# Optimization experiments

Hardware: AMD Instinct MI355X
Metric: run time of the kernel (lower is better)

The kernel has to match this reference:

```python
import math
import jax, jax.numpy as jnp
import numpy as np

B, Q, L, H = 32, 40, 1024, 1024
WINDOW_FRAMES, MAX_V_L = 16, 1024
MAX_DELTA = 0.1
NUM_PASSES = 2


def setup_inputs() -> dict:
    key = jax.random.key(0)
    ks = jax.random.split(key, 8)
    init_log_sigma = math.log(WINDOW_FRAMES / (2.0 * MAX_V_L))
    return {
        "pred_spans": jax.random.uniform(ks[0], (B, Q, 2), dtype=jnp.float32),
        "vid_feat": jax.random.normal(ks[1], (B, L, H), dtype=jnp.float32),
        "vid_mask": jnp.ones((B, L), dtype=jnp.float32),
        "txt_rep": jax.random.normal(ks[2], (B, H), dtype=jnp.float32),
        "log_sigma_start": jnp.float32(init_log_sigma),
        "log_sigma_end": jnp.float32(init_log_sigma),
        "sigma_width_scale_start": jnp.float32(0.01),
        "sigma_width_scale_end": jnp.float32(-0.01),
        "txt_proj_w": jax.random.normal(ks[3], (H, 2), dtype=jnp.float32) * 0.02,
        "txt_proj_b": jnp.zeros((2,), dtype=jnp.float32),
        "mlp0_w": jax.random.normal(ks[4], (3 * H, H), dtype=jnp.float32) * (1.0 / math.sqrt(3 * H)),
        "mlp0_b": jnp.zeros((H,), dtype=jnp.float32),
        "mlp1_w": jax.random.normal(ks[5], (H, 2), dtype=jnp.float32) * (1.0 / math.sqrt(H)),
        "mlp1_b": jnp.zeros((2,), dtype=jnp.float32),
    }


def reference(pred_spans, vid_feat, vid_mask, txt_rep,
              log_sigma_start, log_sigma_end,
              sigma_width_scale_start, sigma_width_scale_end,
              txt_proj_w, txt_proj_b, mlp0_w, mlp0_b, mlp1_w, mlp1_b):
    b, q, _ = pred_spans.shape
    l = vid_feat.shape[1]
    # span (center,width) -> (start,end) in [0,1]
    start = jnp.clip(pred_spans[..., 0] - pred_spans[..., 1] / 2, 0.0, 1.0)  # (B,Q)
    end = jnp.clip(pred_spans[..., 0] + pred_spans[..., 1] / 2, 0.0, 1.0)
    t_pos = jnp.linspace(0.0, 1.0, l)  # (L,)
    min_sig = 1.0 / (4.0 * l)
    log_range = math.log(max(float(l) * min_sig * 4.0, 1.0 + 1e-6))
    # semantic sigma offsets (B,2)
    txt_off = jnp.tanh(txt_rep @ txt_proj_w + txt_proj_b) * (0.5 * log_range)
    txt_off_s, txt_off_e = txt_off[:, 0:1], txt_off[:, 1:2]  # (B,1)
    txt_expand = jnp.broadcast_to(txt_rep[:, None, :], (b, q, txt_rep.shape[-1]))
    mask = vid_mask[:, None, :]  # (B,1,L)

    def _pool(anchor, sigma):
        # Gaussian soft-attention pooling over frames; anchor,sigma: (B,Q)
        dist2 = ((t_pos[None, None, :] - anchor[:, :, None]) / sigma[:, :, None]) ** 2
        w = jnp.exp(-0.5 * dist2) * mask  # (B,Q,L)
        w = w / jnp.maximum(jnp.sum(w, -1, keepdims=True), 1e-8)
        return jnp.einsum('bql,blh->bqh', w, vid_feat)

    passes = []
    for _ in range(NUM_PASSES):
        width = jnp.maximum(end - start, 1e-6)  # (B,Q)
        sig_s = jnp.maximum(jnp.exp(log_sigma_start + sigma_width_scale_start * width + txt_off_s), min_sig)
        sig_e = jnp.maximum(jnp.exp(log_sigma_end + sigma_width_scale_end * width + txt_off_e), min_sig)
        start_feat = _pool(start, sig_s)
        end_feat = _pool(end, sig_e)
        joint = jnp.concatenate([start_feat, end_feat, txt_expand], axis=-1)  # (B,Q,3H)
        hidden = jax.nn.relu(joint @ mlp0_w + mlp0_b)
        deltas = jnp.tanh(hidden @ mlp1_w + mlp1_b) * MAX_DELTA  # (B,Q,2)
        start = jnp.clip(start + deltas[..., 0], 0.0, 1.0)
        end = jnp.clip(end + deltas[..., 1], 0.0, 1.0)
        center_r = (start + end) / 2.0
        width_r = jnp.maximum(end - start, 1e-6)
        passes.append(jnp.stack([center_r, width_r], axis=-1))
    return passes[-1], jnp.stack(passes, axis=0)
```

## Files before the change

### kernel.cpp

```cpp
#include <hip/hip_runtime.h>

#define B_   32
#define Q_   40
#define L_   1024
#define H_   1024
#define QQ_  80
#define M_   1280
#define K3_  3072
#define JK_  2048

#define OB_W0T   0u
#define OB_WT2   6291456u
#define OB_JOINT 11534336u
#define OB_PART  16777216u
#define OB_TXTB  27262976u
#define OB_TXTP  27328512u
#define OB_MISC  27590656u
#define MS_START 0
#define MS_END   1280
#define MS_TOS   2560
#define MS_TOE   2592

typedef short bf8 __attribute__((ext_vector_type(8)));
typedef short bf4 __attribute__((ext_vector_type(4)));
typedef float f4  __attribute__((ext_vector_type(4)));

static __device__ __forceinline__ unsigned short f2b(float f) {
    unsigned int x = __float_as_uint(f);
    unsigned int r = x + 0x7FFFu + ((x >> 16) & 1u);
    return (unsigned short)(r >> 16);
}
static __device__ __forceinline__ unsigned int pk2(float lo, float hi) {
    return (unsigned int)f2b(lo) | ((unsigned int)f2b(hi) << 16);
}
static __device__ __forceinline__ float b2f16(unsigned short u) {
    return __uint_as_float((unsigned int)u << 16);
}
static __device__ __forceinline__ float blo(unsigned int u) {
    return __uint_as_float(u << 16);
}
static __device__ __forceinline__ float bhi(unsigned int u) {
    return __uint_as_float(u & 0xffff0000u);
}

static __device__ __forceinline__ void block_reduce2(float& a, float& b, float* scr) {
    #pragma unroll
    for (int off = 32; off > 0; off >>= 1) {
        a += __shfl_down(a, off);
        b += __shfl_down(b, off);
    }
    int wv = threadIdx.x >> 6, lane = threadIdx.x & 63;
    __syncthreads();
    if (lane == 0) { scr[wv] = a; scr[4 + wv] = b; }
    __syncthreads();
    a = scr[0] + scr[1] + scr[2] + scr[3];
    b = scr[4] + scr[5] + scr[6] + scr[7];
}

__global__ __launch_bounds__(256) void k_setup(const float* __restrict__ w0,
                                               unsigned short* __restrict__ w0t,
                                               const float* __restrict__ txt,
                                               const float* __restrict__ pw,
                                               const float* __restrict__ pb,
                                               const float* __restrict__ spans,
                                               unsigned short* __restrict__ txtb,
                                               float* __restrict__ msc) {
    int z = blockIdx.z, tid = threadIdx.x;
    if (z == 3) {
        int flat = blockIdx.x * 16 + blockIdx.y;
        if (flat < B_) {
            int b = flat;
            int h4 = tid * 4;
            float4 tv = *(const float4*)(txt + (size_t)b * H_ + h4);
            float4 pa = *(const float4*)(pw + 2 * h4);
            float4 pc = *(const float4*)(pw + 2 * h4 + 4);
            float s0 = tv.x * pa.x + tv.y * pa.z + tv.z * pc.x + tv.w * pc.z;
            float s1 = tv.x * pa.y + tv.y * pa.w + tv.z * pc.y + tv.w * pc.w;
            ushort4 o;
            o.x = f2b(tv.x); o.y = f2b(tv.y); o.z = f2b(tv.z); o.w = f2b(tv.w);
            *(ushort4*)(txtb + (size_t)b * H_ + h4) = o;
            __shared__ float scr[8];
            block_reduce2(s0, s1, scr);
            if (tid == 0) {
                const float half_lr = 4.9999975e-07f;
                msc[MS_TOS + b] = tanhf(s0 + pb[0]) * half_lr;
                msc[MS_TOE + b] = tanhf(s1 + pb[1]) * half_lr;
            }
        } else if (flat < 37) {
            int i = (flat - B_) * 256 + tid;
            if (i < M_) {
                float c = spans[2 * i], w = spans[2 * i + 1];
                msc[MS_START + i] = fminf(fmaxf(c - 0.5f * w, 0.f), 1.f);
                msc[MS_END + i]   = fminf(fmaxf(c + 0.5f * w, 0.f), 1.f);
            }
        }
        return;
    }
    __shared__ float tile[64][69];
    const float* s = w0 + (size_t)z * 1024 * H_;
    unsigned short* d = w0t + (size_t)z * 1024;
    int r0 = blockIdx.x * 64, c0 = blockIdx.y * 64;
    int col4 = (tid & 15) * 4, row = tid >> 4;
    #pragma unroll
    for (int it = 0; it < 4; it++) {
        int r = it * 16 + row;
        float4 v = *(const float4*)(s + (size_t)(r0 + r) * 1024 + c0 + col4);
        *(float4*)(&tile[r][col4]) = v;
    }
    __syncthreads();
    #pragma unroll
    for (int it = 0; it < 2; it++) {
        int slot = it * 256 + tid;
        int c = slot >> 3, chunk = slot & 7;
        int r = chunk * 8;
        uint4 vv;
        vv.x = (unsigned int)f2b(tile[r + 0][c]) | ((unsigned int)f2b(tile[r + 1][c]) << 16);
        vv.y = (unsigned int)f2b(tile[r + 2][c]) | ((unsigned int)f2b(tile[r + 3][c]) << 16);
        vv.z = (unsigned int)f2b(tile[r + 4][c]) | ((unsigned int)f2b(tile[r + 5][c]) << 16);
        vv.w = (unsigned int)f2b(tile[r + 6][c]) | ((unsigned int)f2b(tile[r + 7][c]) << 16);
        *(uint4*)(d + (size_t)(c0 + c) * K3_ + r0 + r) = vv;
    }
}

static __device__ __forceinline__ void weights_body(int m, float s, float e,
                                                    const float* __restrict__ vmask,
                                                    float ls_s, float ls_e,
                                                    float sw_s, float sw_e,
                                                    const float* __restrict__ msc,
                                                    unsigned short* __restrict__ wt2,
                                                    float* scr) {
    int b = m / Q_, q = m - b * Q_;
    int tid = threadIdx.x;
    float width = fmaxf(e - s, 1e-6f);
    const float min_sig = 1.0f / (4.0f * (float)L_);
    float sig_s = fmaxf(expf(ls_s + sw_s * width + msc[MS_TOS + b]), min_sig);
    float sig_e = fmaxf(expf(ls_e + sw_e * width + msc[MS_TOE + b]), min_sig);
    float inv_s = 1.0f / sig_s, inv_e = 1.0f / sig_e;

    float wsv[4], wev[4], sumS = 0.f, sumE = 0.f;
    #pragma unroll
    for (int k = 0; k < 4; k++) {
        int l = tid + k * 256;
        float t = (float)l * (1.0f / 1023.0f);
        float mk = vmask[b * L_ + l];
        float ds = (t - s) * inv_s, de = (t - e) * inv_e;
        float a = expf(-0.5f * ds * ds) * mk;
        float c = expf(-0.5f * de * de) * mk;
        wsv[k] = a; wev[k] = c; sumS += a; sumE += c;
    }
    block_reduce2(sumS, sumE, scr);
    float iS = 1.0f / fmaxf(sumS, 1e-8f);
    float iE = 1.0f / fmaxf(sumE, 1e-8f);
    unsigned short* wq = wt2 + ((size_t)b * QQ_ + q) * L_;
    unsigned short* we = wt2 + ((size_t)b * QQ_ + Q_ + q) * L_;
    #pragma unroll
    for (int k = 0; k < 4; k++) {
        int l = tid + k * 256;
        wq[l] = f2b(wsv[k] * iS);
        we[l] = f2b(wev[k] * iE);
    }
}

__global__ __launch_bounds__(256) void k_stage2(const float* __restrict__ vmask,
                                                const float* __restrict__ p_ls_s,
                                                const float* __restrict__ p_ls_e,
                                                const float* __restrict__ p_sw_s,
                                                const float* __restrict__ p_sw_e,
                                                const float* __restrict__ msc,
                                                unsigned short* __restrict__ wt2,
                                                const unsigned short* __restrict__ txtb,
                                                const unsigned short* __restrict__ w0t,
                                                unsigned short* __restrict__ txtp) {
    int bid = blockIdx.x;
    if (bid < M_) {
        __shared__ float scr[8];
        int m = bid;
        weights_body(m, msc[MS_START + m], msc[MS_END + m], vmask,
                     p_ls_s[0], p_ls_e[0], p_sw_s[0], p_sw_e[0], msc, wt2, scr);
        return;
    }
    int t = bid - M_;
    int nIdx = t & 15, mIdx = (t >> 4) & 1, kIdx = t >> 5;
    int wv = threadIdx.x >> 6, lane = threadIdx.x & 63;
    int ml = lane & 15, kg = lane >> 4;
    int mbase = mIdx * 16;
    int nbase = nIdx * 64 + wv * 16;
    int kz = kIdx * 256;
    const unsigned short* ap = txtb + ((size_t)(mbase + ml) * H_ + kz + kg * 8);
    const unsigned short* bp = w0t + ((size_t)(nbase + ml) * K3_ + JK_ + kz + kg * 8);
    f4 acc = (f4){0.f, 0.f, 0.f, 0.f};
    #pragma unroll
    for (int k0 = 0; k0 < 256; k0 += 32) {
        bf8 a = *(const bf8*)(ap + k0);
        bf8 bb = *(const bf8*)(bp + k0);
        acc = __builtin_amdgcn_mfma_f32_16x16x32_bf16(a, bb, acc, 0, 0, 0);
    }
    unsigned short* pp = txtp + (size_t)kIdx * B_ * H_;
    int n = nbase + ml;
    #pragma unroll
    for (int r = 0; r < 4; r++) {
        int m = mbase + kg * 4 + r;
        pp[(size_t)m * H_ + n] = f2b(acc[r]);
    }
}

__global__ __launch_bounds__(512) void k_pool_mfma(const float* __restrict__ vid,
                                                   const unsigned short* __restrict__ wt2,
                                                   unsigned short* __restrict__ joint) {
    int b = blockIdx.x, ht = blockIdx.y;
    int tid = threadIdx.x;
    int wv = tid >> 6, lane = tid & 63;
    int hsub = wv & 3, half = wv >> 2;
    int ml = lane & 15, kg = lane >> 4;
    int h0 = ht * 64;

    __shared__ __align__(16) unsigned short tb[2][2][2048];
    __shared__ __align__(16) unsigned short ta[2][2][80 * 40];
    __shared__ float cmb[80][68];

    int st = tid & 255;
    int sl = st >> 3;
    int sh8 = (st & 7) * 8;
    int b_off = ((((sh8 >> 4) * 2 + ((sl >> 2) & 1)) * 4 + (sl >> 3)) * 4 + (sl & 3)) * 16
                + (sh8 & 15);
    const float* vbase = vid + ((size_t)b * L_ + half * 512) * H_ + h0;
    const unsigned short* awsrc = wt2 + (size_t)b * QQ_ * L_ + half * 512;

    f4 acc[5];
    #pragma unroll
    for (int t = 0; t < 5; t++) acc[t] = (f4){0.f, 0.f, 0.f, 0.f};

    auto stage = [&](int c, int buf) {
        const float* src = vbase + (size_t)(c * 32 + sl) * H_ + sh8;
        float4 v0 = *(const float4*)(src);
        float4 v1 = *(const float4*)(src + 4);
        uint4 w;
        w.x = pk2(v0.x, v0.y);
        w.y = pk2(v0.z, v0.w);
        w.z = pk2(v1.x, v1.y);
        w.w = pk2(v1.z, v1.w);
        *(uint4*)(&tb[half][buf][b_off]) = w;
        {
            int row = st >> 2, seg = (st & 3) * 8;
            uint4 av = *(const uint4*)(awsrc + (size_t)row * L_ + c * 32 + seg);
            *(uint4*)(&ta[half][buf][row * 40 + seg]) = av;
        }
        if (st < 64) {
            int i = st + 256;
            int row = i >> 2, seg = (i & 3) * 8;
            uint4 av = *(const uint4*)(awsrc + (size_t)row * L_ + c * 32 + seg);
            *(uint4*)(&ta[half][buf][row * 40 + seg]) = av;
        }
    };

    stage(0, 0);
    __syncthreads();

    for (int c = 0; c < 16; c++) {
        int buf = c & 1;
        if (c < 15) stage(c + 1, buf ^ 1);

        unsigned trb = (unsigned)(uintptr_t)(&tb[half][buf][0]) + hsub * 1024 + lane * 8;
        bf4 lo, hi;
        asm volatile("ds_read_b64_tr_b16 %0, %2\n\t"
                     "ds_read_b64_tr_b16 %1, %2 offset:512\n\t"
                     "s_waitcnt lgkmcnt(0)"
                     : "=v"(lo), "=v"(hi)
                     : "v"(trb));
        __builtin_amdgcn_sched_barrier(0);
        bf8 bfrag = __builtin_shufflevector(lo, hi, 0, 1, 2, 3, 4, 5, 6, 7);

        #pragma unroll
        for (int t = 0; t < 5; t++) {
            bf8 afr = *(const bf8*)(&ta[half][buf][(t * 16 + ml) * 40 + kg * 8]);
            acc[t] = __builtin_amdgcn_mfma_f32_16x16x32_bf16(afr, bfrag, acc[t], 0, 0, 0);
        }
        __syncthreads();
    }

    if (half == 1) {
        #pragma unroll
        for (int t = 0; t < 5; t++)
            #pragma unroll
            for (int r = 0; r < 4; r++)
                cmb[t * 16 + kg * 4 + r][hsub * 16 + ml] = acc[t][r];
    }
    __syncthreads();
    if (half == 0) {
        #pragma unroll
        for (int t = 0; t < 5; t++)
            #pragma unroll
            for (int r = 0; r < 4; r++)
                cmb[t * 16 + kg * 4 + r][hsub * 16 + ml] += acc[t][r];
    }
    __syncthreads();
    for (int idx = tid; idx < 640; idx += 512) {
        int qq = idx >> 3, h8 = (idx & 7) * 8;
        const float* cr = &cmb[qq][h8];
        uint4 vv;
        vv.x = pk2(cr[0], cr[1]);
        vv.y = pk2(cr[2], cr[3]);
        vv.z = pk2(cr[4], cr[5]);
        vv.w = pk2(cr[6], cr[7]);
        int row = b * Q_ + (qq >= Q_ ? qq - Q_ : qq);
        int col = (qq >= Q_ ? H_ : 0) + h0 + h8;
        *(uint4*)(joint + (size_t)row * JK_ + col) = vv;
    }
}

__global__ __launch_bounds__(256) void k_mlp0_mfma(const unsigned short* __restrict__ joint,
                                                   const unsigned short* __restrict__ w0t,
                                                   const unsigned short* __restrict__ txtp,
                                                   unsigned short* __restrict__ part) {
    int wv = threadIdx.x >> 6, lane = threadIdx.x & 63;
    int ml = lane & 15, kg = lane >> 4;
    int mbase = blockIdx.x * 64 + wv * 16;
    int nbase = blockIdx.y * 64;
    int kbase = blockIdx.z * 512;
    const unsigned short* ap = joint + ((size_t)(mbase + ml) * JK_ + kbase + kg * 8);
    const unsigned short* bp = w0t + ((size_t)(nbase + ml) * K3_ + kbase + kg * 8);
    f4 acc[4];
    #pragma unroll
    for (int t = 0; t < 4; t++) acc[t] = (f4){0.f, 0.f, 0.f, 0.f};

    #pragma unroll 4
    for (int k0 = 0; k0 < 512; k0 += 32) {
        bf8 a = *(const bf8*)(ap + k0);
        #pragma unroll
        for (int t = 0; t < 4; t++) {
            bf8 bb = *(const bf8*)(bp + (size_t)t * 16 * K3_ + k0);
            acc[t] = __builtin_amdgcn_mfma_f32_16x16x32_bf16(a, bb, acc[t], 0, 0, 0);
        }
    }
    const unsigned short* tp = txtp + (size_t)blockIdx.z * B_ * H_;
    unsigned short* pp = part + (size_t)blockIdx.z * M_ * H_;
    #pragma unroll
    for (int t = 0; t < 4; t++) {
        int n = nbase + t * 16 + ml;
        #pragma unroll
        for (int r = 0; r < 4; r++) {
            int m = mbase + kg * 4 + r;
            int b = m / Q_;
            float v = acc[t][r] + b2f16(tp[(size_t)b * H_ + n]);
            pp[(size_t)m * H_ + n] = f2b(v);
        }
    }
}

__global__ __launch_bounds__(256) void k_mlp1w(const float* __restrict__ w1,
                                               const float* __restrict__ b0,
                                               const float* __restrict__ b1,
                                               const unsigned short* __restrict__ part,
                                               float* __restrict__ msc,
                                               float* __restrict__ out, int pass,
                                               int do_weights,
                                               const float* __restrict__ vmask,
                                               const float* __restrict__ p_ls_s,
                                               const float* __restrict__ p_ls_e,
                                               const float* __restrict__ p_sw_s,
                                               const float* __restrict__ p_sw_e,
                                               unsigned short* __restrict__ wt2) {
    int m = blockIdx.x, tid = threadIdx.x;
    int k4 = tid * 4;
    float4 bb = *(const float4*)(b0 + k4);
    float h0 = bb.x, h1 = bb.y, h2 = bb.z, h3 = bb.w;
    #pragma unroll
    for (int z = 0; z < 4; z++) {
        uint2 u = *(const uint2*)(part + (size_t)z * M_ * H_ + (size_t)m * H_ + k4);
        h0 += blo(u.x); h1 += bhi(u.x);
        h2 += blo(u.y); h3 += bhi(u.y);
    }
    h0 = fmaxf(h0, 0.f); h1 = fmaxf(h1, 0.f);
    h2 = fmaxf(h2, 0.f); h3 = fmaxf(h3, 0.f);
    float4 wa = *(const float4*)(w1 + 2 * k4);
    float4 wb = *(const float4*)(w1 + 2 * k4 + 4);
    float p0 = h0 * wa.x + h1 * wa.z + h2 * wb.x + h3 * wb.z;
    float p1 = h0 * wa.y + h1 * wa.w + h2 * wb.y + h3 * wb.w;

    __shared__ float scr[8];
    __shared__ float sh_s, sh_e;
    block_reduce2(p0, p1, scr);
    if (tid == 0) {
        float d0 = tanhf(p0 + b1[0]) * 0.1f;
        float d1 = tanhf(p1 + b1[1]) * 0.1f;
        float s = fminf(fmaxf(msc[MS_START + m] + d0, 0.f), 1.f);
        float e = fminf(fmaxf(msc[MS_END + m] + d1, 0.f), 1.f);
        msc[MS_START + m] = s;
        msc[MS_END + m] = e;
        sh_s = s; sh_e = e;
        float cen = 0.5f * (s + e);
        float wid = fmaxf(e - s, 1e-6f);
        out[2560 + (size_t)(pass * M_ + m) * 2 + 0] = cen;
        out[2560 + (size_t)(pass * M_ + m) * 2 + 1] = wid;
        if (pass == 1) { out[2 * m + 0] = cen; out[2 * m + 1] = wid; }
    }
    __syncthreads();
    if (do_weights) {
        weights_body(m, sh_s, sh_e, vmask,
                     p_ls_s[0], p_ls_e[0], p_sw_s[0], p_sw_e[0], msc, wt2, scr);
    }
}

extern "C" void kernel_launch(void* const* d_in, const int* in_sizes, int n_in,
                              void* d_out, int out_size, void* d_ws, size_t ws_size,
                              hipStream_t stream) {
    const float* spans = (const float*)d_in[0];
    const float* vid   = (const float*)d_in[1];
    const float* vmask = (const float*)d_in[2];
    const float* txt   = (const float*)d_in[3];
    const float* ls_s  = (const float*)d_in[4];
    const float* ls_e  = (const float*)d_in[5];
    const float* sw_s  = (const float*)d_in[6];
    const float* sw_e  = (const float*)d_in[7];
    const float* pw    = (const float*)d_in[8];
    const float* pb    = (const float*)d_in[9];
    const float* w0    = (const float*)d_in[10];
    const float* b0    = (const float*)d_in[11];
    const float* w1    = (const float*)d_in[12];
    const float* b1    = (const float*)d_in[13];
    char* wsb = (char*)d_ws;
    unsigned short* w0t   = (unsigned short*)(wsb + OB_W0T);
    unsigned short* wt2   = (unsigned short*)(wsb + OB_WT2);
    unsigned short* joint = (unsigned short*)(wsb + OB_JOINT);
    unsigned short* part  = (unsigned short*)(wsb + OB_PART);
    unsigned short* txtb  = (unsigned short*)(wsb + OB_TXTB);
    unsigned short* txtp  = (unsigned short*)(wsb + OB_TXTP);
    float* msc = (float*)(wsb + OB_MISC);
    float* out = (float*)d_out;

    hipLaunchKernelGGL(k_setup, dim3(16, 16, 4), dim3(256), 0, stream,
                       w0, w0t, txt, pw, pb, spans, txtb, msc);
    hipLaunchKernelGGL(k_stage2, dim3(M_ + 128), dim3(256), 0, stream,
                       vmask, ls_s, ls_e, sw_s, sw_e, msc, wt2, txtb, w0t, txtp);
    for (int p = 0; p < 2; p++) {
        hipLaunchKernelGGL(k_pool_mfma, dim3(B_, 16), dim3(512), 0, stream, vid, wt2, joint);
        hipLaunchKernelGGL(k_mlp0_mfma, dim3(20, 16, 4), dim3(256), 0, stream,
                           joint, w0t, txtp, part);
        hipLaunchKernelGGL(k_mlp1w, dim3(M_), dim3(256), 0, stream,
                           w1, b0, b1, part, msc, out, p, (p == 0) ? 1 : 0,
                           vmask, ls_s, ls_e, sw_s, sw_e, wt2);
    }
}
```

Before: 364.0 us.

## Restructure pooling kernel to single K-split with register-prefetched 64-frame chunks

The pooling GEMM drops the two-half K split across 512 threads in favour of 256 threads that each cover the full L dimension, using 64-frame chunks. Global loads for the next chunk go into registers before the MFMAs and are written to LDS afterwards, so memory latency overlaps compute. This also removes the shared-memory cross-half reduction and its extra barriers, writing results straight from the accumulators. The trade-off is fewer waves per block for hiding latency, more registers per thread, and uncoalesced scalar bf16 stores to joint.

```diff
diff --git a/kernel.cpp b/kernel.cpp
--- a/kernel.cpp
+++ b/kernel.cpp
@@ -204,107 +204,108 @@
     }
 }
 
-__global__ __launch_bounds__(512) void k_pool_mfma(const float* __restrict__ vid,
+__global__ __launch_bounds__(256) void k_pool_mfma(const float* __restrict__ vid,
                                                    const unsigned short* __restrict__ wt2,
                                                    unsigned short* __restrict__ joint) {
     int b = blockIdx.x, ht = blockIdx.y;
     int tid = threadIdx.x;
-    int wv = tid >> 6, lane = tid & 63;
-    int hsub = wv & 3, half = wv >> 2;
+    int hsub = tid >> 6, lane = tid & 63;
     int ml = lane & 15, kg = lane >> 4;
     int h0 = ht * 64;
 
-    __shared__ __align__(16) unsigned short tb[2][2][2048];
-    __shared__ __align__(16) unsigned short ta[2][2][80 * 40];
-    __shared__ float cmb[80][68];
-
-    int st = tid & 255;
-    int sl = st >> 3;
-    int sh8 = (st & 7) * 8;
-    int b_off = ((((sh8 >> 4) * 2 + ((sl >> 2) & 1)) * 4 + (sl >> 3)) * 4 + (sl & 3)) * 16
-                + (sh8 & 15);
-    const float* vbase = vid + ((size_t)b * L_ + half * 512) * H_ + h0;
-    const unsigned short* awsrc = wt2 + (size_t)b * QQ_ * L_ + half * 512;
+    __shared__ __align__(16) unsigned short tb[2][4096];
+    __shared__ __align__(16) unsigned short ta[2][80 * 72];
+
+    int l0 = tid >> 3;
+    int h8 = (tid & 7) * 8;
+    int sB = (l0 >> 2) & 1, kgB = l0 >> 3, lrB = l0 & 3;
+    int h16 = h8 >> 4, hc = h8 & 15;
+    int b_off = ((((h16) * 2 + sB) * 4 + kgB) * 64) + lrB * 16 + hc;
+    const float* vbase = vid + (size_t)b * L_ * H_ + h0 + h8;
+
+    const unsigned short* awsrc = wt2 + (size_t)b * QQ_ * L_;
 
     f4 acc[5];
     #pragma unroll
     for (int t = 0; t < 5; t++) acc[t] = (f4){0.f, 0.f, 0.f, 0.f};
 
-    auto stage = [&](int c, int buf) {
-        const float* src = vbase + (size_t)(c * 32 + sl) * H_ + sh8;
-        float4 v0 = *(const float4*)(src);
-        float4 v1 = *(const float4*)(src + 4);
+    float4 pv0, pv1, pv2, pv3;
+    uint4 av0, av1, av2;
+
+    auto issueB = [&](int c) {
+        const float* src = vbase + (size_t)(c * 64 + l0) * H_;
+        pv0 = *(const float4*)(src);
+        pv1 = *(const float4*)(src + 4);
+        pv2 = *(const float4*)(src + 32 * H_);
+        pv3 = *(const float4*)(src + 32 * H_ + 4);
+    };
+    auto issueA = [&](int c) {
+        int i0 = tid, i1 = tid + 256;
+        av0 = *(const uint4*)(awsrc + (size_t)(i0 >> 3) * L_ + c * 64 + (i0 & 7) * 8);
+        av1 = *(const uint4*)(awsrc + (size_t)(i1 >> 3) * L_ + c * 64 + (i1 & 7) * 8);
+        if (tid < 128) {
+            int i2 = tid + 512;
+            av2 = *(const uint4*)(awsrc + (size_t)(i2 >> 3) * L_ + c * 64 + (i2 & 7) * 8);
+        }
+    };
+    auto writeStage = [&](int buf) {
         uint4 w;
-        w.x = pk2(v0.x, v0.y);
-        w.y = pk2(v0.z, v0.w);
-        w.z = pk2(v1.x, v1.y);
-        w.w = pk2(v1.z, v1.w);
-        *(uint4*)(&tb[half][buf][b_off]) = w;
-        {
-            int row = st >> 2, seg = (st & 3) * 8;
-            uint4 av = *(const uint4*)(awsrc + (size_t)row * L_ + c * 32 + seg);
-            *(uint4*)(&ta[half][buf][row * 40 + seg]) = av;
-        }
-        if (st < 64) {
-            int i = st + 256;
-            int row = i >> 2, seg = (i & 3) * 8;
-            uint4 av = *(const uint4*)(awsrc + (size_t)row * L_ + c * 32 + seg);
-            *(uint4*)(&ta[half][buf][row * 40 + seg]) = av;
+        w.x = pk2(pv0.x, pv0.y); w.y = pk2(pv0.z, pv0.w);
+        w.z = pk2(pv1.x, pv1.y); w.w = pk2(pv1.z, pv1.w);
+        *(uint4*)(&tb[buf][b_off]) = w;
+        uint4 w2;
+        w2.x = pk2(pv2.x, pv2.y); w2.y = pk2(pv2.z, pv2.w);
+        w2.z = pk2(pv3.x, pv3.y); w2.w = pk2(pv3.z, pv3.w);
+        *(uint4*)(&tb[buf][b_off + 2048]) = w2;
+        int i0 = tid, i1 = tid + 256;
+        *(uint4*)(&ta[buf][(i0 >> 3) * 72 + (i0 & 7) * 8]) = av0;
+        *(uint4*)(&ta[buf][(i1 >> 3) * 72 + (i1 & 7) * 8]) = av1;
+        if (tid < 128) {
+            int i2 = tid + 512;
+            *(uint4*)(&ta[buf][(i2 >> 3) * 72 + (i2 & 7) * 8]) = av2;
         }
     };
 
-    stage(0, 0);
+    issueB(0); issueA(0);
+    writeStage(0);
     __syncthreads();
 
     for (int c = 0; c < 16; c++) {
         int buf = c & 1;
-        if (c < 15) stage(c + 1, buf ^ 1);
-
-        unsigned trb = (unsigned)(uintptr_t)(&tb[half][buf][0]) + hsub * 1024 + lane * 8;
-        bf4 lo, hi;
-        asm volatile("ds_read_b64_tr_b16 %0, %2\n\t"
-                     "ds_read_b64_tr_b16 %1, %2 offset:512\n\t"
-                     "s_waitcnt lgkmcnt(0)"
-                     : "=v"(lo), "=v"(hi)
-                     : "v"(trb));
-        __builtin_amdgcn_sched_barrier(0);
-        bf8 bfrag = __builtin_shufflevector(lo, hi, 0, 1, 2, 3, 4, 5, 6, 7);
+        if (c < 15) { issueB(c + 1); issueA(c + 1); }
 
         #pragma unroll
-        for (int t = 0; t < 5; t++) {
-            bf8 afr = *(const bf8*)(&ta[half][buf][(t * 16 + ml) * 40 + kg * 8]);
-            acc[t] = __builtin_amdgcn_mfma_f32_16x16x32_bf16(afr, bfrag, acc[t], 0, 0, 0);
-        }
+        for (int s2 = 0; s2 < 2; s2++) {
+            unsigned trb = (unsigned)(uintptr_t)(&tb[buf][0]) + (s2 * 4 + hsub) * 1024
+                           + lane * 8;
+            bf4 lo, hi;
+            asm volatile("ds_read_b64_tr_b16 %0, %2\n\t"
+                         "ds_read_b64_tr_b16 %1, %2 offset:512\n\t"
+                         "s_waitcnt lgkmcnt(0)"
+                         : "=v"(lo), "=v"(hi)
+                         : "v"(trb));
+            __builtin_amdgcn_sched_barrier(0);
+            bf8 bfrag = __builtin_shufflevector(lo, hi, 0, 1, 2, 3, 4, 5, 6, 7);
+            #pragma unroll
+            for (int t = 0; t < 5; t++) {
+                bf8 afr = *(const bf8*)(&ta[buf][(t * 16 + ml) * 72 + s2 * 32 + kg * 8]);
+                acc[t] = __builtin_amdgcn_mfma_f32_16x16x32_bf16(afr, bfrag, acc[t], 0, 0, 0);
+            }
+        }
+
+        if (c < 15) writeStage(buf ^ 1);
         __syncthreads();
     }
 
-    if (half == 1) {
+    #pragma unroll
+    for (int t = 0; t < 5; t++) {
         #pragma unroll
-        for (int t = 0; t < 5; t++)
-            #pragma unroll
-            for (int r = 0; r < 4; r++)
-                cmb[t * 16 + kg * 4 + r][hsub * 16 + ml] = acc[t][r];
-    }
-    __syncthreads();
-    if (half == 0) {
-        #pragma unroll
-        for (int t = 0; t < 5; t++)
-            #pragma unroll
-            for (int r = 0; r < 4; r++)
-                cmb[t * 16 + kg * 4 + r][hsub * 16 + ml] += acc[t][r];
-    }
-    __syncthreads();
-    for (int idx = tid; idx < 640; idx += 512) {
-        int qq = idx >> 3, h8 = (idx & 7) * 8;
-        const float* cr = &cmb[qq][h8];
-        uint4 vv;
-        vv.x = pk2(cr[0], cr[1]);
-        vv.y = pk2(cr[2], cr[3]);
-        vv.z = pk2(cr[4], cr[5]);
-        vv.w = pk2(cr[6], cr[7]);
-        int row = b * Q_ + (qq >= Q_ ? qq - Q_ : qq);
-        int col = (qq >= Q_ ? H_ : 0) + h0 + h8;
-        *(uint4*)(joint + (size_t)row * JK_ + col) = vv;
+        for (int r = 0; r < 4; r++) {
+            int qq = t * 16 + kg * 4 + r;
+            int row = b * Q_ + (qq >= Q_ ? qq - Q_ : qq);
+            int col = (qq >= Q_ ? H_ : 0) + h0 + hsub * 16 + ml;
+            joint[(size_t)row * JK_ + col] = f2b(acc[t][r]);
+        }
     }
 }
 
@@ -433,7 +434,7 @@
     hipLaunchKernelGGL(k_stage2, dim3(M_ + 128), dim3(256), 0, stream,
                        vmask, ls_s, ls_e, sw_s, sw_e, msc, wt2, txtb, w0t, txtp);
     for (int p = 0; p < 2; p++) {
-        hipLaunchKernelGGL(k_pool_mfma, dim3(B_, 16), dim3(512), 0, stream, vid, wt2, joint);
+        hipLaunchKernelGGL(k_pool_mfma, dim3(B_, 16), dim3(256), 0, stream, vid, wt2, joint);
         hipLaunchKernelGGL(k_mlp0_mfma, dim3(20, 16, 4), dim3(256), 0, stream,
                            joint, w0t, txtp, part);
         hipLaunchKernelGGL(k_mlp1w, dim3(M_), dim3(256), 0, stream,
```

Result: no change. 365.1 us (+0.3%).
